# Optimization experiments

Measured on AMD Instinct MI355X. Metric: run time of the kernel, lower is better.

Reference implementation:

```python
import jax, jax.numpy as jnp
import numpy as np

D_HIDDEN = 1024
N_HEADS = 16
D_HEAD = 64
B, N = 4, 1024
EPS = 1e-5


def _lin(x, w, b):
    # torch Linear: y = x @ W^T + b, w: [out, in]
    return jnp.einsum('...i,oi->...o', x, w) + b


def _ln(x, g, b):
    m = jnp.mean(x, axis=-1, keepdims=True)
    v = jnp.mean(jnp.square(x - m), axis=-1, keepdims=True)
    return (x - m) * jax.lax.rsqrt(v + EPS) * g + b


def setup_inputs() -> dict:
    key = jax.random.key(0)
    ks = jax.random.split(key, 20)
    d = D_HIDDEN
    s = 0.02
    inp = {
        'x': jax.random.normal(ks[0], (B, N, d), jnp.float32),
        'time_emb': jax.random.normal(ks[1], (B, d), jnp.float32),
        'ln1_g': jnp.ones((d,), jnp.float32),
        'ln1_b': jnp.zeros((d,), jnp.float32),
        's1_w': jax.random.normal(ks[2], (d, d), jnp.float32) * s,
        's1_b': jnp.zeros((d,), jnp.float32),
        'o1_w': jax.random.normal(ks[3], (d, d), jnp.float32) * s,
        'o1_b': jnp.zeros((d,), jnp.float32),
        'qkv_w': jax.random.normal(ks[4], (3 * d, d), jnp.float32) * s,
        'qkv_b': jnp.zeros((3 * d,), jnp.float32),
        'proj_w': jax.random.normal(ks[5], (d, d), jnp.float32) * s,
        'proj_b': jnp.zeros((d,), jnp.float32),
        'ln2_g': jnp.ones((d,), jnp.float32),
        'ln2_b': jnp.zeros((d,), jnp.float32),
        's2_w': jax.random.normal(ks[6], (d, d), jnp.float32) * s,
        's2_b': jnp.zeros((d,), jnp.float32),
        'o2_w': jax.random.normal(ks[7], (d, d), jnp.float32) * s,
        'o2_b': jnp.zeros((d,), jnp.float32),
        'up_w': jax.random.normal(ks[8], (4 * d, d), jnp.float32) * s,
        'up_b': jnp.zeros((4 * d,), jnp.float32),
        'down_w': jax.random.normal(ks[9], (d, 4 * d), jnp.float32) * s,
        'down_b': jnp.zeros((d,), jnp.float32),
    }
    return inp


def reference(x, time_emb, ln1_g, ln1_b, s1_w, s1_b, o1_w, o1_b,
              qkv_w, qkv_b, proj_w, proj_b, ln2_g, ln2_b,
              s2_w, s2_b, o2_w, o2_b, up_w, up_b, down_w, down_b):
    d = D_HIDDEN

    def ada(h, sw, sb, ow, ob):
        scale = _lin(time_emb, sw, sb)[:, None, :]   # [B,1,d]
        offset = _lin(time_emb, ow, ob)[:, None, :]
        return (1.0 + scale) * h + offset

    # attention branch
    h = ada(_ln(x, ln1_g, ln1_b), s1_w, s1_b, o1_w, o1_b)
    qkv = _lin(h, qkv_w, qkv_b)                       # [B,N,3d]
    q, k, v = jnp.split(qkv, 3, axis=-1)
    q = q.reshape(B, N, N_HEADS, D_HEAD)
    k = k.reshape(B, N, N_HEADS, D_HEAD)
    v = v.reshape(B, N, N_HEADS, D_HEAD)
    wei = jnp.einsum('bnhd,bmhd->bhnm', q, k) * (D_HEAD ** -0.5)
    wei = jax.nn.softmax(wei, axis=-1)
    attn = jnp.einsum('bhnm,bmhd->bnhd', wei, v).reshape(B, N, d)
    x = x + _lin(attn, proj_w, proj_b)

    # mlp branch (torch nn.GELU default = exact erf gelu)
    h = ada(_ln(x, ln2_g, ln2_b), s2_w, s2_b, o2_w, o2_b)
    h = jax.nn.gelu(_lin(h, up_w, up_b), approximate=False)
    x = x + _lin(h, down_w, down_b)
    return x, time_emb
```

## Files before the change

kernel.cpp:

```cpp
#include <hip/hip_runtime.h>
#include <hip/hip_bf16.h>
#include <math.h>

#define DH 1024
#define BB 4
#define NN 1024
#define NH 16
#define HD 64

typedef __attribute__((ext_vector_type(8))) short bf16x8;
typedef __attribute__((ext_vector_type(4))) float f32x4;
typedef unsigned short u16;

static __device__ __forceinline__ u16 f2bf(float f) {
  __hip_bfloat16 h = __float2bfloat16(f);
  return *reinterpret_cast<u16*>(&h);
}
static __device__ __forceinline__ float bf2f(u16 x) {
  return __uint_as_float((unsigned)x << 16);
}

#define MFMA16(a, b, c) __builtin_amdgcn_mfma_f32_16x16x32_bf16(a, b, c, 0, 0, 0)
#define VMCNT(n) asm volatile("s_waitcnt vmcnt(" #n ")" ::: "memory")
#define MEMFENCE asm volatile("" ::: "memory")
#define BAR() do { __builtin_amdgcn_s_barrier(); MEMFENCE; } while (0)

static __device__ __forceinline__ void async16(const void* g, void* l) {
  __builtin_amdgcn_global_load_lds(
      (const __attribute__((address_space(1))) void*)g,
      (__attribute__((address_space(3))) void*)l, 16, 0, 0);
}

__global__ void cvt_all_kernel(const float* __restrict__ wq, const float* __restrict__ wp,
                               const float* __restrict__ wu, const float* __restrict__ wd,
                               u16* __restrict__ oq, u16* __restrict__ op,
                               u16* __restrict__ ou, u16* __restrict__ od) {
  int i = blockIdx.x * 256 + threadIdx.x;
  const float* src; u16* dst; int off;
  if (i < 786432)            { src = wq; dst = oq; off = i; }
  else if (i < 1048576)      { src = wp; dst = op; off = i - 786432; }
  else if (i < 2097152)      { src = wu; dst = ou; off = i - 1048576; }
  else                       { src = wd; dst = od; off = i - 2097152; }
  float4 v = reinterpret_cast<const float4*>(src)[off];
  ushort4 o;
  o.x = f2bf(v.x); o.y = f2bf(v.y); o.z = f2bf(v.z); o.w = f2bf(v.w);
  reinterpret_cast<ushort4*>(dst)[off] = o;
}

__global__ __launch_bounds__(256) void adaln_kernel(
    const float* __restrict__ e,
    const float* __restrict__ w_s1, const float* __restrict__ b_s1,
    const float* __restrict__ w_o1, const float* __restrict__ b_o1,
    const float* __restrict__ w_s2, const float* __restrict__ b_s2,
    const float* __restrict__ w_o2, const float* __restrict__ b_o2,
    float* __restrict__ out) {
  int tid = threadIdx.x, wid = tid >> 6, lane = tid & 63;
  int mat = blockIdx.y;
  const float* w; const float* bs; float addc;
  if (mat == 0)      { w = w_s1; bs = b_s1; addc = 1.f; }
  else if (mat == 1) { w = w_o1; bs = b_o1; addc = 0.f; }
  else if (mat == 2) { w = w_s2; bs = b_s2; addc = 1.f; }
  else               { w = w_o2; bs = b_o2; addc = 0.f; }
  int col = blockIdx.x * 4 + wid;
  float a0 = 0.f, a1 = 0.f, a2 = 0.f, a3 = 0.f;
  const float* wc_ = w + (size_t)col * DH;
  for (int i = 0; i < 16; ++i) {
    int k = i * 64 + lane;
    float wv = wc_[k];
    a0 += wv * e[k];
    a1 += wv * e[DH + k];
    a2 += wv * e[2 * DH + k];
    a3 += wv * e[3 * DH + k];
  }
  #pragma unroll
  for (int msk = 32; msk; msk >>= 1) {
    a0 += __shfl_xor(a0, msk); a1 += __shfl_xor(a1, msk);
    a2 += __shfl_xor(a2, msk); a3 += __shfl_xor(a3, msk);
  }
  if (lane == 0) {
    float bb = bs[col] + addc;
    out[mat * (4 * DH) + 0 * DH + col] = a0 + bb;
    out[mat * (4 * DH) + 1 * DH + col] = a1 + bb;
    out[mat * (4 * DH) + 2 * DH + col] = a2 + bb;
    out[mat * (4 * DH) + 3 * DH + col] = a3 + bb;
  }
}

__global__ __launch_bounds__(256) void ln_mod_kernel(
    const float* __restrict__ x, const float* __restrict__ g, const float* __restrict__ bta,
    const float* __restrict__ sp, const float* __restrict__ off, u16* __restrict__ out) {
  int row = blockIdx.x;
  int b = row >> 10;
  int tid = threadIdx.x;
  int wid = tid >> 6, lane = tid & 63;
  const float4 xv = reinterpret_cast<const float4*>(x + (size_t)row * DH)[tid];
  float s = xv.x + xv.y + xv.z + xv.w;
  float ss = xv.x * xv.x + xv.y * xv.y + xv.z * xv.z + xv.w * xv.w;
  #pragma unroll
  for (int m = 32; m; m >>= 1) { s += __shfl_xor(s, m); ss += __shfl_xor(ss, m); }
  __shared__ float red[8];
  if (lane == 0) { red[wid] = s; red[4 + wid] = ss; }
  __syncthreads();
  s = red[0] + red[1] + red[2] + red[3];
  ss = red[4] + red[5] + red[6] + red[7];
  float mean = s * (1.f / DH);
  float var = ss * (1.f / DH) - mean * mean;
  float rstd = rsqrtf(var + 1e-5f);
  int c = tid * 4;
  const float* spb = sp + b * DH + c;
  const float* offb = off + b * DH + c;
  float y0 = (xv.x - mean) * rstd * g[c + 0] + bta[c + 0];
  float y1 = (xv.y - mean) * rstd * g[c + 1] + bta[c + 1];
  float y2 = (xv.z - mean) * rstd * g[c + 2] + bta[c + 2];
  float y3 = (xv.w - mean) * rstd * g[c + 3] + bta[c + 3];
  ushort4 o;
  o.x = f2bf(spb[0] * y0 + offb[0]);
  o.y = f2bf(spb[1] * y1 + offb[1]);
  o.z = f2bf(spb[2] * y2 + offb[2]);
  o.w = f2bf(spb[3] * y3 + offb[3]);
  reinterpret_cast<ushort4*>(out + (size_t)row * DH)[tid] = o;
}

enum { EPI_BF16 = 0, EPI_GELU = 1, EPI_PART = 2 };

template <int EPI>
__global__ __launch_bounds__(512, 2) void gemmT_kernel(
    const u16* __restrict__ A, const u16* __restrict__ W,
    const float* __restrict__ bias, void* __restrict__ outp,
    int N, int K, int KT) {
  extern __shared__ u16 lds[];
  u16* Ab = lds;
  u16* Bb = lds + 16384;
  int tid = threadIdx.x;
  int wid = tid >> 6, lane = tid & 63;
  int l15 = lane & 15, l4 = lane >> 4;
  int wr = wid >> 2, wc = wid & 3;

  int nwg = gridDim.x * gridDim.y;
  int lin = blockIdx.y * gridDim.x + blockIdx.x;
  int q8 = nwg >> 3;
  int lin2 = (lin & 7) * q8 + (lin >> 3);
  int bx = lin2 % gridDim.x, by = lin2 / gridDim.x;
  int m0 = by * 256, n0 = bx * 128;
  int k0 = blockIdx.z * (KT << 5);

  f32x4 acc[8][2] = {};

  const u16* Abase = A + (size_t)m0 * K + k0;
  const u16* Wbase = W + (size_t)n0 * K + k0;
  int i0 = tid, i1 = 512 + tid;
  int r0 = i0 >> 2, c0 = (i0 & 3) ^ ((r0 >> 1) & 3);
  int r1 = i1 >> 2, c1 = (i1 & 3) ^ ((r1 >> 1) & 3);
  int rB = tid >> 2, cB = (tid & 3) ^ ((rB >> 1) & 3);
  size_t gA0 = (size_t)r0 * K + c0 * 8;
  size_t gA1 = (size_t)r1 * K + c1 * 8;
  size_t gB0 = (size_t)rB * K + cB * 8;
  int lbA0 = (wid * 64) * 8;
  int lbA1 = (512 + wid * 64) * 8;

  auto stage = [&](int tt) {
    int qa = (tt & 1) * 8192, qb = (tt & 1) * 4096;
    const u16* Ak = Abase + tt * 32;
    const u16* Wk = Wbase + tt * 32;
    async16(Ak + gA0, &Ab[qa + lbA0]);
    async16(Ak + gA1, &Ab[qa + lbA1]);
    async16(Wk + gB0, &Bb[qb + lbA0]);
  };

  auto compute = [&](int tt) {
    int qa = (tt & 1) * 8192, qb = (tt & 1) * 4096;
    bf16x8 af[8], bfr[2];
    #pragma unroll
    for (int m = 0; m < 8; ++m) {
      int row = wr * 128 + m * 16 + l15;
      int ps = l4 ^ ((row >> 1) & 3);
      af[m] = *reinterpret_cast<const bf16x8*>(&Ab[qa + row * 32 + ps * 8]);
    }
    #pragma unroll
    for (int n = 0; n < 2; ++n) {
      int row = wc * 32 + n * 16 + l15;
      int ps = l4 ^ ((row >> 1) & 3);
      bfr[n] = *reinterpret_cast<const bf16x8*>(&Bb[qb + row * 32 + ps * 8]);
    }
    #pragma unroll
    for (int m = 0; m < 8; ++m)
      #pragma unroll
      for (int n = 0; n < 2; ++n)
        acc[m][n] = MFMA16(af[m], bfr[n], acc[m][n]);
  };

  stage(0);
  for (int t = 0; t < KT; ++t) {
    if (t < KT - 1) { stage(t + 1); VMCNT(3); }
    else { VMCNT(0); }
    BAR();
    compute(t);
    MEMFENCE;
    BAR();
  }

  int M = gridDim.y * 256;
  u16* pout = (u16*)outp + (size_t)blockIdx.z * M * N;
  #pragma unroll
  for (int n = 0; n < 2; ++n) {
    int col = n0 + wc * 32 + n * 16 + l15;
    float bv = (EPI == EPI_PART) ? 0.f : bias[col];
    #pragma unroll
    for (int m = 0; m < 8; ++m) {
      #pragma unroll
      for (int r = 0; r < 4; ++r) {
        int rowg = m0 + wr * 128 + m * 16 + l4 * 4 + r;
        float v = acc[m][n][r] + bv;
        if (EPI == EPI_GELU) {
          v = 0.5f * v * (1.f + erff(v * 0.70710678118f));
          ((u16*)outp)[(size_t)rowg * N + col] = f2bf(v);
        } else if (EPI == EPI_BF16) {
          ((u16*)outp)[(size_t)rowg * N + col] = f2bf(v);
        } else {
          pout[(size_t)rowg * N + col] = f2bf(v);
        }
      }
    }
  }
}

enum { OEPI_BF16 = 0, OEPI_GELU = 1, OEPI_RES = 2 };

template <int EPI>
__global__ __launch_bounds__(256, 3) void gemm_bt_kernel(
    const u16* __restrict__ A, const u16* __restrict__ W,
    const float* __restrict__ bias, const float* __restrict__ resid,
    void* __restrict__ outp, int N, int K) {
  __shared__ __align__(16) u16 As[2][128 * 32];
  __shared__ __align__(16) u16 Ws[2][128 * 32];
  int tid = threadIdx.x;
  int wid = tid >> 6, lane = tid & 63;
  int l15 = lane & 15, l4 = lane >> 4;
  int m0 = blockIdx.y * 128, n0 = blockIdx.x * 128;
  int wr = wid >> 1, wc = wid & 1;
  f32x4 acc[4][4] = {};

  const int KT = K >> 5;
  int idx0 = tid, idx1 = 256 + tid;
  int rowA0 = idx0 >> 2, gs0 = (idx0 & 3) ^ ((rowA0 >> 1) & 3);
  int rowA1 = idx1 >> 2, gs1 = (idx1 & 3) ^ ((rowA1 >> 1) & 3);
  const u16* Abase = A + (size_t)m0 * K;
  const u16* Wbase = W + (size_t)n0 * K;
  int lb0 = (wid * 64) * 8;
  int lb1 = (256 + wid * 64) * 8;

  auto stage = [&](int buf, int kt) {
    const u16* Ak = Abase + kt * 32;
    const u16* Wk = Wbase + kt * 32;
    async16(Ak + (size_t)rowA0 * K + gs0 * 8, &As[buf][lb0]);
    async16(Wk + (size_t)rowA0 * K + gs0 * 8, &Ws[buf][lb0]);
    async16(Ak + (size_t)rowA1 * K + gs1 * 8, &As[buf][lb1]);
    async16(Wk + (size_t)rowA1 * K + gs1 * 8, &Ws[buf][lb1]);
  };

  auto compute = [&](int buf) {
    bf16x8 af[4], wf[4];
    #pragma unroll
    for (int m = 0; m < 4; ++m) {
      int row = wr * 64 + m * 16 + l15;
      int ps = l4 ^ ((row >> 1) & 3);
      af[m] = *reinterpret_cast<const bf16x8*>(&As[buf][row * 32 + ps * 8]);
    }
    #pragma unroll
    for (int n = 0; n < 4; ++n) {
      int row = wc * 64 + n * 16 + l15;
      int ps = l4 ^ ((row >> 1) & 3);
      wf[n] = *reinterpret_cast<const bf16x8*>(&Ws[buf][row * 32 + ps * 8]);
    }
    #pragma unroll
    for (int m = 0; m < 4; ++m)
      #pragma unroll
      for (int n = 0; n < 4; ++n)
        acc[m][n] = MFMA16(af[m], wf[n], acc[m][n]);
  };

  stage(0, 0);
  __syncthreads();
  int buf = 0;
  for (int kt = 0; kt < KT - 1; ++kt) {
    stage(buf ^ 1, kt + 1);
    compute(buf);
    __syncthreads();
    buf ^= 1;
  }
  compute(buf);

  #pragma unroll
  for (int n = 0; n < 4; ++n) {
    int col = n0 + wc * 64 + n * 16 + l15;
    float bv = bias[col];
    #pragma unroll
    for (int m = 0; m < 4; ++m) {
      #pragma unroll
      for (int r = 0; r < 4; ++r) {
        int rowg = m0 + wr * 64 + m * 16 + l4 * 4 + r;
        float v = acc[m][n][r] + bv;
        if (EPI == OEPI_GELU) {
          v = 0.5f * v * (1.f + erff(v * 0.70710678118f));
          ((u16*)outp)[(size_t)rowg * N + col] = f2bf(v);
        } else if (EPI == OEPI_BF16) {
          ((u16*)outp)[(size_t)rowg * N + col] = f2bf(v);
        } else {
          ((float*)outp)[(size_t)rowg * N + col] = v + resid[(size_t)rowg * N + col];
        }
      }
    }
  }
}

__global__ __launch_bounds__(256) void reduce4_kernel(
    const u16* __restrict__ part, const float* __restrict__ x2,
    const float* __restrict__ bias, const float* __restrict__ te,
    float* __restrict__ out) {
  size_t i = (size_t)blockIdx.x * 256 + threadIdx.x;
  const size_t MN = (size_t)4096 * 1024;
  float4 xr = reinterpret_cast<const float4*>(x2)[i];
  int col = (int)((i * 4) & 1023);
  float4 bv = *reinterpret_cast<const float4*>(&bias[col]);
  float a0 = xr.x + bv.x, a1 = xr.y + bv.y, a2 = xr.z + bv.z, a3 = xr.w + bv.w;
  #pragma unroll
  for (int p = 0; p < 4; ++p) {
    ushort4 u = reinterpret_cast<const ushort4*>(part + p * MN)[i];
    a0 += bf2f(u.x); a1 += bf2f(u.y); a2 += bf2f(u.z); a3 += bf2f(u.w);
  }
  float4 o; o.x = a0; o.y = a1; o.z = a2; o.w = a3;
  reinterpret_cast<float4*>(out)[i] = o;
  if (blockIdx.x < 16) {
    int ii = blockIdx.x * 256 + threadIdx.x;
    out[4096 * 1024 + ii] = te[ii];
  }
}

__global__ __launch_bounds__(256) void vt_kernel(const u16* __restrict__ qkvb,
                                                 u16* __restrict__ vT) {
  __shared__ u16 L[64 * 66];
  int bh = blockIdx.y;
  int b = bh >> 4, h = bh & 15;
  int nt = blockIdx.x;
  int t = threadIdx.x;
  const u16* src = qkvb + ((size_t)b * 1024 + nt * 64) * 3072 + 2048 + h * 64;
  int j = t >> 3, s = t & 7;
  bf16x8 r0 = *reinterpret_cast<const bf16x8*>(src + (size_t)j * 3072 + s * 8);
  bf16x8 r1 = *reinterpret_cast<const bf16x8*>(src + (size_t)(j + 32) * 3072 + s * 8);
  #pragma unroll
  for (int e = 0; e < 8; ++e) {
    L[(s * 8 + e) * 66 + j] = r0[e];
    L[(s * 8 + e) * 66 + j + 32] = r1[e];
  }
  __syncthreads();
  int d = t & 63, cp = t >> 6;
  u16* dst = vT + ((size_t)bh * 64 + d) * 1024 + nt * 64;
  #pragma unroll
  for (int half = 0; half < 2; ++half) {
    int cs = cp + half * 4;
    bf16x8 o;
    #pragma unroll
    for (int c = 0; c < 8; ++c) o[c] = L[d * 66 + cs * 8 + c];
    *reinterpret_cast<bf16x8*>(dst + cs * 8) = o;
  }
}

__global__ __launch_bounds__(256, 4) void attn_kernel(
    const u16* __restrict__ qkv, const u16* __restrict__ vT, u16* __restrict__ out) {
  __shared__ __align__(16) u16 Ks[2][4096];
  __shared__ __align__(16) u16 Vs[2][4096];
  __shared__ __align__(16) u16 Ps[4][1024];
  int tid = threadIdx.x, wid = tid >> 6, lane = tid & 63;
  int l15 = lane & 15, l4 = lane >> 4;
  int L = blockIdx.y * gridDim.x + blockIdx.x;
  int qt = (L >> 3) & 15;
  int bh = (L & 7) | ((L >> 7) << 3);
  int b = bh >> 4, h = bh & 15;
  const size_t SN = 3 * DH;
  const u16* qb = qkv + (size_t)b * NN * SN + h * HD;
  const u16* kb = qb + DH;
  const u16* vtb = vT + (size_t)bh * 64 * 1024;

  int qrow = qt * 64 + wid * 16 + l15;
  bf16x8 qf[2];
  #pragma unroll
  for (int ks = 0; ks < 2; ++ks)
    qf[ks] = *reinterpret_cast<const bf16x8*>(qb + (size_t)qrow * SN + ks * 32 + l4 * 8);

  float m_[4], l_[4];
  f32x4 o_[4] = {};
  #pragma unroll
  for (int r = 0; r < 4; ++r) { m_[r] = -1e30f; l_[r] = 0.f; }

  int iA = tid, iB = 256 + tid;
  int jA = iA >> 3, sA = iA & 7, gsA = sA ^ (jA & 7);
  int jB = iB >> 3, sB = iB & 7, gsB = sB ^ (jB & 7);

  auto stageKV = [&](int bufn, int t) {
    const u16* kt = kb + (size_t)t * 64 * SN;
    async16(kt + (size_t)jA * SN + gsA * 8, &Ks[bufn][iA * 8]);
    async16(kt + (size_t)jB * SN + gsB * 8, &Ks[bufn][iB * 8]);
    const u16* vt = vtb + (size_t)t * 64;
    async16(vt + (size_t)jA * 1024 + gsA * 8, &Vs[bufn][iA * 8]);
    async16(vt + (size_t)jB * 1024 + gsB * 8, &Vs[bufn][iB * 8]);
  };

  stageKV(0, 0);
  __syncthreads();

  int buf = 0;
  for (int t = 0; t < 16; ++t) {
    if (t < 15) stageKV(buf ^ 1, t + 1);

    f32x4 sa[4];
    #pragma unroll
    for (int nb = 0; nb < 4; ++nb) {
      f32x4 s = {};
      #pragma unroll
      for (int ks = 0; ks < 2; ++ks) {
        int j = nb * 16 + l15;
        int ps = (ks * 4 + l4) ^ (j & 7);
        bf16x8 kf = *reinterpret_cast<const bf16x8*>(&Ks[buf][j * 64 + ps * 8]);
        s = MFMA16(qf[ks], kf, s);
      }
      sa[nb] = s * 0.125f;
    }

    float rm[4], tsum[4];
    #pragma unroll
    for (int r = 0; r < 4; ++r) {
      float v = fmaxf(fmaxf(sa[0][r], sa[1][r]), fmaxf(sa[2][r], sa[3][r]));
      #pragma unroll
      for (int msk = 1; msk < 16; msk <<= 1) v = fmaxf(v, __shfl_xor(v, msk));
      rm[r] = v;
    }
    float gmx = fmaxf(fmaxf(rm[0] - m_[0], rm[1] - m_[1]),
                      fmaxf(rm[2] - m_[2], rm[3] - m_[3]));
    if (!__all(gmx <= 8.f)) {
      #pragma unroll
      for (int r = 0; r < 4; ++r) {
        float mn = fmaxf(m_[r], rm[r]);
        float corr = __expf(m_[r] - mn);
        m_[r] = mn;
        l_[r] *= corr;
        #pragma unroll
        for (int nd = 0; nd < 4; ++nd) o_[nd][r] *= corr;
      }
    }
    #pragma unroll
    for (int r = 0; r < 4; ++r) tsum[r] = 0.f;
    #pragma unroll
    for (int nb = 0; nb < 4; ++nb) {
      #pragma unroll
      for (int r = 0; r < 4; ++r) {
        float p = __expf(sa[nb][r] - m_[r]);
        sa[nb][r] = p;
        tsum[r] += p;
      }
    }
    #pragma unroll
    for (int r = 0; r < 4; ++r) {
      float v = tsum[r];
      #pragma unroll
      for (int msk = 1; msk < 16; msk <<= 1) v += __shfl_xor(v, msk);
      l_[r] += v;
    }

    u16* Pw = Ps[wid];
    #pragma unroll
    for (int nb = 0; nb < 4; ++nb) {
      int slot = nb * 2 + (l15 >> 3);
      #pragma unroll
      for (int r = 0; r < 4; ++r) {
        int row = l4 * 4 + r;
        int ps = slot ^ (row & 7);
        Pw[row * 64 + ps * 8 + (l15 & 7)] = f2bf(sa[nb][r]);
      }
    }

    __builtin_amdgcn_s_setprio(1);
    #pragma unroll
    for (int ks = 0; ks < 2; ++ks) {
      int psp = (ks * 4 + l4) ^ (l15 & 7);
      bf16x8 pa = *reinterpret_cast<const bf16x8*>(&Pw[l15 * 64 + psp * 8]);
      #pragma unroll
      for (int nd = 0; nd < 4; ++nd) {
        int d = nd * 16 + l15;
        int psv = (ks * 4 + l4) ^ (d & 7);
        bf16x8 vf = *reinterpret_cast<const bf16x8*>(&Vs[buf][d * 64 + psv * 8]);
        o_[nd] = MFMA16(pa, vf, o_[nd]);
      }
    }
    __builtin_amdgcn_s_setprio(0);

    if (t < 15) __syncthreads();
    buf ^= 1;
  }

  float inv[4];
  #pragma unroll
  for (int r = 0; r < 4; ++r) inv[r] = 1.f / l_[r];
  u16* ob = out + (size_t)b * NN * DH + h * HD;
  #pragma unroll
  for (int nd = 0; nd < 4; ++nd) {
    #pragma unroll
    for (int r = 0; r < 4; ++r) {
      int q = qt * 64 + wid * 16 + l4 * 4 + r;
      ob[(size_t)q * DH + nd * 16 + l15] = f2bf(o_[nd][r] * inv[r]);
    }
  }
}

extern "C" void kernel_launch(void* const* d_in, const int* in_sizes, int n_in,
                              void* d_out, int out_size, void* d_ws, size_t ws_size,
                              hipStream_t stream) {
  (void)in_sizes; (void)n_in; (void)out_size; (void)ws_size;
  const float* x      = (const float*)d_in[0];
  const float* te     = (const float*)d_in[1];
  const float* ln1_g  = (const float*)d_in[2];
  const float* ln1_b  = (const float*)d_in[3];
  const float* s1_w   = (const float*)d_in[4];
  const float* s1_b   = (const float*)d_in[5];
  const float* o1_w   = (const float*)d_in[6];
  const float* o1_b   = (const float*)d_in[7];
  const float* qkv_w  = (const float*)d_in[8];
  const float* qkv_b  = (const float*)d_in[9];
  const float* proj_w = (const float*)d_in[10];
  const float* proj_b = (const float*)d_in[11];
  const float* ln2_g  = (const float*)d_in[12];
  const float* ln2_b  = (const float*)d_in[13];
  const float* s2_w   = (const float*)d_in[14];
  const float* s2_b   = (const float*)d_in[15];
  const float* o2_w   = (const float*)d_in[16];
  const float* o2_b   = (const float*)d_in[17];
  const float* up_w   = (const float*)d_in[18];
  const float* up_b   = (const float*)d_in[19];
  const float* down_w = (const float*)d_in[20];
  const float* down_b = (const float*)d_in[21];

  char* ws = (char*)d_ws;
  size_t off = 0;
  auto alloc = [&](size_t bytes) { void* p = ws + off; off += (bytes + 255) & ~255ull; return p; };
  u16*   wq   = (u16*)  alloc((size_t)3072 * 1024 * 2);
  u16*   wp   = (u16*)  alloc((size_t)1024 * 1024 * 2);
  u16*   wu   = (u16*)  alloc((size_t)4096 * 1024 * 2);
  u16*   h1   = (u16*)  alloc((size_t)4096 * 1024 * 2);
  u16*   qkvb = (u16*)  alloc((size_t)4096 * 3072 * 2);
  u16*   att  = (u16*)  alloc((size_t)4096 * 1024 * 2);
  u16*   h2   = (u16*)  alloc((size_t)4096 * 1024 * 2);
  u16*   wd   = (u16*)  alloc((size_t)1024 * 4096 * 2);
  float* x2   = (float*)alloc((size_t)4096 * 1024 * 4);
  u16*   upb  = (u16*)  alloc((size_t)4096 * 4096 * 2);
  float* ada  = (float*)alloc((size_t)4 * 4 * 1024 * 4);
  float* sp1 = ada, *off1 = ada + 4096, *sp2 = ada + 8192, *off2 = ada + 12288;
  u16*   part = wq;
  u16*   vT   = h1;

  cvt_all_kernel<<<12288, 256, 0, stream>>>(qkv_w, proj_w, up_w, down_w, wq, wp, wu, wd);
  adaln_kernel<<<dim3(256, 4), 256, 0, stream>>>(te, s1_w, s1_b, o1_w, o1_b, s2_w, s2_b, o2_w, o2_b, ada);
  ln_mod_kernel<<<4096, 256, 0, stream>>>(x, ln1_g, ln1_b, sp1, off1, h1);
  gemmT_kernel<EPI_BF16><<<dim3(24, 16, 1), 512, 49152, stream>>>(h1, wq, qkv_b, qkvb, 3072, 1024, 32);
  vt_kernel<<<dim3(16, 64), 256, 0, stream>>>(qkvb, vT);
  attn_kernel<<<dim3(16, 64), 256, 0, stream>>>(qkvb, vT, att);
  gemm_bt_kernel<OEPI_RES><<<dim3(8, 32), 256, 0, stream>>>(att, wp, proj_b, x, x2, 1024, 1024);
  ln_mod_kernel<<<4096, 256, 0, stream>>>(x2, ln2_g, ln2_b, sp2, off2, h2);
  gemmT_kernel<EPI_GELU><<<dim3(32, 16, 1), 512, 49152, stream>>>(h2, wu, up_b, upb, 4096, 1024, 32);
  gemmT_kernel<EPI_PART><<<dim3(8, 16, 4), 512, 49152, stream>>>(upb, wd, nullptr, part, 1024, 4096, 32);
  reduce4_kernel<<<4096, 256, 0, stream>>>(part, x2, down_b, te, (float*)d_out);
}
```

Before: 267.1 us.

## Transpose QK^T MFMA so softmax runs per-lane and P stays in registers

Swaps the MFMA operand order for S = QK^T so each lane holds scores for a single query row. The row max and sum then need only two cross-lane shuffles instead of per-row 16-lane butterflies. The P tile is packed to bf16 and redistributed into the A-operand layout with register shuffles, removing the per-wave LDS round trip for P. In exchange it adds shuffles for the rescale factors and for the P redistribution, and the LDS footprint drops.

```diff
diff --git a/kernel.cpp b/kernel.cpp
--- a/kernel.cpp
+++ b/kernel.cpp
@@ -10,7 +10,9 @@
 
 typedef __attribute__((ext_vector_type(8))) short bf16x8;
 typedef __attribute__((ext_vector_type(4))) float f32x4;
+typedef __attribute__((ext_vector_type(4))) unsigned int u32x4;
 typedef unsigned short u16;
+typedef unsigned int u32;
 
 static __device__ __forceinline__ u16 f2bf(float f) {
   __hip_bfloat16 h = __float2bfloat16(f);
@@ -369,7 +371,6 @@
     const u16* __restrict__ qkv, const u16* __restrict__ vT, u16* __restrict__ out) {
   __shared__ __align__(16) u16 Ks[2][4096];
   __shared__ __align__(16) u16 Vs[2][4096];
-  __shared__ __align__(16) u16 Ps[4][1024];
   int tid = threadIdx.x, wid = tid >> 6, lane = tid & 63;
   int l15 = lane & 15, l4 = lane >> 4;
   int L = blockIdx.y * gridDim.x + blockIdx.x;
@@ -387,10 +388,12 @@
   for (int ks = 0; ks < 2; ++ks)
     qf[ks] = *reinterpret_cast<const bf16x8*>(qb + (size_t)qrow * SN + ks * 32 + l4 * 8);
 
-  float m_[4], l_[4];
+  float m_ = -1e30f, l_ = 0.f;
   f32x4 o_[4] = {};
-  #pragma unroll
-  for (int r = 0; r < 4; ++r) { m_[r] = -1e30f; l_[r] = 0.f; }
+
+  int laA = ((l4 * 2) & 3) * 16 + l15;
+  int laB = ((l4 * 2 + 1) & 3) * 16 + l15;
+  bool nbhi = (l4 >> 1) != 0;
 
   int iA = tid, iB = 256 + tid;
   int jA = iA >> 3, sA = iA & 7, gsA = sA ^ (jA & 7);
@@ -421,68 +424,65 @@
         int j = nb * 16 + l15;
         int ps = (ks * 4 + l4) ^ (j & 7);
         bf16x8 kf = *reinterpret_cast<const bf16x8*>(&Ks[buf][j * 64 + ps * 8]);
-        s = MFMA16(qf[ks], kf, s);
+        s = MFMA16(kf, qf[ks], s);
       }
       sa[nb] = s * 0.125f;
     }
 
-    float rm[4], tsum[4];
-    #pragma unroll
-    for (int r = 0; r < 4; ++r) {
-      float v = fmaxf(fmaxf(sa[0][r], sa[1][r]), fmaxf(sa[2][r], sa[3][r]));
-      #pragma unroll
-      for (int msk = 1; msk < 16; msk <<= 1) v = fmaxf(v, __shfl_xor(v, msk));
-      rm[r] = v;
-    }
-    float gmx = fmaxf(fmaxf(rm[0] - m_[0], rm[1] - m_[1]),
-                      fmaxf(rm[2] - m_[2], rm[3] - m_[3]));
-    if (!__all(gmx <= 8.f)) {
-      #pragma unroll
-      for (int r = 0; r < 4; ++r) {
-        float mn = fmaxf(m_[r], rm[r]);
-        float corr = __expf(m_[r] - mn);
-        m_[r] = mn;
-        l_[r] *= corr;
-        #pragma unroll
-        for (int nd = 0; nd < 4; ++nd) o_[nd][r] *= corr;
+    float pm = sa[0][0];
+    #pragma unroll
+    for (int nb = 0; nb < 4; ++nb)
+      #pragma unroll
+      for (int r = 0; r < 4; ++r)
+        if (nb || r) pm = fmaxf(pm, sa[nb][r]);
+    pm = fmaxf(pm, __shfl_xor(pm, 16));
+    pm = fmaxf(pm, __shfl_xor(pm, 32));
+
+    if (!__all(pm - m_ <= 8.f)) {
+      float mn = fmaxf(m_, pm);
+      float corr = __expf(m_ - mn);
+      m_ = mn;
+      l_ *= corr;
+      float c0 = __shfl(corr, l4 * 4 + 0);
+      float c1 = __shfl(corr, l4 * 4 + 1);
+      float c2 = __shfl(corr, l4 * 4 + 2);
+      float c3 = __shfl(corr, l4 * 4 + 3);
+      #pragma unroll
+      for (int nd = 0; nd < 4; ++nd) {
+        o_[nd][0] *= c0; o_[nd][1] *= c1; o_[nd][2] *= c2; o_[nd][3] *= c3;
       }
     }
-    #pragma unroll
-    for (int r = 0; r < 4; ++r) tsum[r] = 0.f;
+
+    float ts = 0.f;
+    u32 pk[4][2];
     #pragma unroll
     for (int nb = 0; nb < 4; ++nb) {
-      #pragma unroll
-      for (int r = 0; r < 4; ++r) {
-        float p = __expf(sa[nb][r] - m_[r]);
-        sa[nb][r] = p;
-        tsum[r] += p;
-      }
-    }
-    #pragma unroll
-    for (int r = 0; r < 4; ++r) {
-      float v = tsum[r];
-      #pragma unroll
-      for (int msk = 1; msk < 16; msk <<= 1) v += __shfl_xor(v, msk);
-      l_[r] += v;
-    }
-
-    u16* Pw = Ps[wid];
-    #pragma unroll
-    for (int nb = 0; nb < 4; ++nb) {
-      int slot = nb * 2 + (l15 >> 3);
-      #pragma unroll
-      for (int r = 0; r < 4; ++r) {
-        int row = l4 * 4 + r;
-        int ps = slot ^ (row & 7);
-        Pw[row * 64 + ps * 8 + (l15 & 7)] = f2bf(sa[nb][r]);
-      }
-    }
+      float p0 = __expf(sa[nb][0] - m_);
+      float p1 = __expf(sa[nb][1] - m_);
+      float p2 = __expf(sa[nb][2] - m_);
+      float p3 = __expf(sa[nb][3] - m_);
+      ts += (p0 + p1) + (p2 + p3);
+      pk[nb][0] = (u32)f2bf(p0) | ((u32)f2bf(p1) << 16);
+      pk[nb][1] = (u32)f2bf(p2) | ((u32)f2bf(p3) << 16);
+    }
+    ts += __shfl_xor(ts, 16);
+    ts += __shfl_xor(ts, 32);
+    l_ += ts;
 
     __builtin_amdgcn_s_setprio(1);
     #pragma unroll
     for (int ks = 0; ks < 2; ++ks) {
-      int psp = (ks * 4 + l4) ^ (l15 & 7);
-      bf16x8 pa = *reinterpret_cast<const bf16x8*>(&Pw[l15 * 64 + psp * 8]);
+      int nlo = ks * 2, nhi = ks * 2 + 1;
+      u32 a00 = __shfl((int)pk[nlo][0], laA), a01 = __shfl((int)pk[nlo][1], laA);
+      u32 a10 = __shfl((int)pk[nhi][0], laA), a11 = __shfl((int)pk[nhi][1], laA);
+      u32 b00 = __shfl((int)pk[nlo][0], laB), b01 = __shfl((int)pk[nlo][1], laB);
+      u32 b10 = __shfl((int)pk[nhi][0], laB), b11 = __shfl((int)pk[nhi][1], laB);
+      u32x4 wv;
+      wv[0] = nbhi ? a10 : a00;
+      wv[1] = nbhi ? a11 : a01;
+      wv[2] = nbhi ? b10 : b00;
+      wv[3] = nbhi ? b11 : b01;
+      bf16x8 pa = __builtin_bit_cast(bf16x8, wv);
       #pragma unroll
       for (int nd = 0; nd < 4; ++nd) {
         int d = nd * 16 + l15;
@@ -497,9 +497,11 @@
     buf ^= 1;
   }
 
-  float inv[4];
-  #pragma unroll
-  for (int r = 0; r < 4; ++r) inv[r] = 1.f / l_[r];
+  float li0 = __shfl(l_, l4 * 4 + 0);
+  float li1 = __shfl(l_, l4 * 4 + 1);
+  float li2 = __shfl(l_, l4 * 4 + 2);
+  float li3 = __shfl(l_, l4 * 4 + 3);
+  float inv[4] = { 1.f / li0, 1.f / li1, 1.f / li2, 1.f / li3 };
   u16* ob = out + (size_t)b * NN * DH + h * HD;
   #pragma unroll
   for (int nd = 0; nd < 4; ++nd) {
```

Result: faster. 252.1 us (-5.6%).
